# Kernel tuning notes

Hardware: AMD Instinct MI355X
Metric: run time of the kernel (lower is better)

The kernel has to match this reference:

```python
import jax, jax.numpy as jnp
import numpy as np

B, L, C, H = 8, 2048, 1024, 16
HID = 4 * C


def _rope(x):
    # Faithful to source: rotation angle depends only on feature index (no position scaling).
    b, n, c = x.shape
    k_max = c // 2
    theta = 1.0 / (10000.0 ** (jnp.arange(k_max, dtype=jnp.float32) / k_max))
    cos_t, sin_t = jnp.cos(theta), jnp.sin(theta)
    xr = x.reshape(b, n, k_max, 2)
    re = xr[..., 0] * cos_t - xr[..., 1] * sin_t
    im = xr[..., 0] * sin_t + xr[..., 1] * cos_t
    return jnp.stack((re, im), axis=-1).reshape(b, n, c)


def _dwconv(x_bcl, w, bias):
    # depthwise conv1d, kernel 3, padding 1; w: (C,1,3)
    y = jax.lax.conv_general_dilated(
        x_bcl, w, (1,), [(1, 1)],
        dimension_numbers=('NCH', 'OIH', 'NCH'),
        feature_group_count=x_bcl.shape[1])
    return y + bias[None, :, None]


def _ln(x, g, b, eps=1e-5):
    mu = x.mean(-1, keepdims=True)
    var = ((x - mu) ** 2).mean(-1, keepdims=True)
    return (x - mu) * jax.lax.rsqrt(var + eps) * g + b


def _mlla_forward(x, cpe1_w, cpe1_b, norm1_g, norm1_b, in_w, in_b, actp_w, actp_b,
                  dwc_w, dwc_b, qk_w, qk_b, lepe_w, lepe_b, out_w, out_b,
                  cpe2_w, cpe2_b, norm2_g, norm2_b, fc1_w, fc1_b, fc2_w, fc2_b):
    b, n, c = x.shape
    h, d = H, c // H
    # cpe1 residual
    x = x + _dwconv(x.transpose(0, 2, 1), cpe1_w, cpe1_b).transpose(0, 2, 1)
    shortcut = x
    xn = _ln(x, norm1_g, norm1_b)
    act_res = jax.nn.silu(xn @ actp_w + actp_b)
    xi = xn @ in_w + in_b
    xi = jax.nn.silu(_dwconv(xi.transpose(0, 2, 1), dwc_w, dwc_b)).transpose(0, 2, 1)
    # linear attention with ELU+1 feature map and RoPE on q/k
    qk = xi @ qk_w + qk_b                       # (b,n,2c)
    q = jax.nn.elu(qk[..., :c]) + 1.0
    k = jax.nn.elu(qk[..., c:]) + 1.0
    q_rope = _rope(q).reshape(b, n, h, d).transpose(0, 2, 1, 3)  # (b,h,n,d)
    k_rope = _rope(k).reshape(b, n, h, d).transpose(0, 2, 1, 3)
    qh = q.reshape(b, n, h, d).transpose(0, 2, 1, 3)
    kh = k.reshape(b, n, h, d).transpose(0, 2, 1, 3)
    vh = xi.reshape(b, n, h, d).transpose(0, 2, 1, 3)
    k_mean = kh.mean(axis=2, keepdims=True)                      # (b,h,1,d)
    z = 1.0 / (jnp.einsum('bhnd,bhmd->bhnm', qh, k_mean) + 1e-6)  # (b,h,n,1)
    kv = jnp.einsum('bhnd,bhne->bhde', k_rope, vh) * (1.0 / n)   # (k*n^-0.5)^T @ (v*n^-0.5)
    attn = jnp.einsum('bhnd,bhde->bhne', q_rope, kv) * z         # (b,h,n,d)
    attn = attn.transpose(0, 2, 1, 3).reshape(b, n, c)
    v_bcl = vh.transpose(0, 2, 1, 3).reshape(b, n, c).transpose(0, 2, 1)
    attn = attn + _dwconv(v_bcl, lepe_w, lepe_b).transpose(0, 2, 1)
    # gated output projection + residual
    x = shortcut + (attn * act_res) @ out_w + out_b
    # cpe2 residual
    x = x + _dwconv(x.transpose(0, 2, 1), cpe2_w, cpe2_b).transpose(0, 2, 1)
    # MLP (exact GELU, as torch default)
    xn2 = _ln(x, norm2_g, norm2_b)
    mlp = jax.nn.gelu(xn2 @ fc1_w + fc1_b, approximate=False) @ fc2_w + fc2_b
    return x + mlp


def setup_inputs() -> dict:
    key = jax.random.key(0)
    ks = jax.random.split(key, 12)
    def nrm(k, shape, scale=0.02):
        return jax.random.normal(k, shape, jnp.float32) * scale
    return {
        'x': jax.random.normal(ks[0], (B, L, C), jnp.float32),
        'cpe1_w': nrm(ks[1], (C, 1, 3), 0.1), 'cpe1_b': jnp.zeros((C,), jnp.float32),
        'norm1_g': jnp.ones((C,), jnp.float32), 'norm1_b': jnp.zeros((C,), jnp.float32),
        'in_w': nrm(ks[2], (C, C)), 'in_b': jnp.zeros((C,), jnp.float32),
        'actp_w': nrm(ks[3], (C, C)), 'actp_b': jnp.zeros((C,), jnp.float32),
        'dwc_w': nrm(ks[4], (C, 1, 3), 0.1), 'dwc_b': jnp.zeros((C,), jnp.float32),
        'qk_w': nrm(ks[5], (C, 2 * C)), 'qk_b': jnp.zeros((2 * C,), jnp.float32),
        'lepe_w': nrm(ks[6], (C, 1, 3), 0.1), 'lepe_b': jnp.zeros((C,), jnp.float32),
        'out_w': nrm(ks[7], (C, C)), 'out_b': jnp.zeros((C,), jnp.float32),
        'cpe2_w': nrm(ks[8], (C, 1, 3), 0.1), 'cpe2_b': jnp.zeros((C,), jnp.float32),
        'norm2_g': jnp.ones((C,), jnp.float32), 'norm2_b': jnp.zeros((C,), jnp.float32),
        'fc1_w': nrm(ks[9], (C, HID)), 'fc1_b': jnp.zeros((HID,), jnp.float32),
        'fc2_w': nrm(ks[10], (HID, C)), 'fc2_b': jnp.zeros((C,), jnp.float32),
    }


def reference(x, cpe1_w, cpe1_b, norm1_g, norm1_b, in_w, in_b, actp_w, actp_b,
              dwc_w, dwc_b, qk_w, qk_b, lepe_w, lepe_b, out_w, out_b,
              cpe2_w, cpe2_b, norm2_g, norm2_b, fc1_w, fc1_b, fc2_w, fc2_b):
    return _mlla_forward(x, cpe1_w, cpe1_b, norm1_g, norm1_b, in_w, in_b, actp_w, actp_b,
                         dwc_w, dwc_b, qk_w, qk_b, lepe_w, lepe_b, out_w, out_b,
                         cpe2_w, cpe2_b, norm2_g, norm2_b, fc1_w, fc1_b, fc2_w, fc2_b)
```

## Files before the change

### kernel.cpp

```cpp
#include <hip/hip_runtime.h>
#include <hip/hip_bf16.h>
#include <cstdint>

#define B_    8
#define L_    2048
#define C_    1024
#define H_    16
#define D_    64
#define BL_   16384
#define C2_   2048
#define HID_  4096
#define KMAX_ 512

typedef unsigned short u16;
typedef unsigned int   u32;
typedef __attribute__((ext_vector_type(8))) short short8;
typedef __attribute__((ext_vector_type(4))) float f32x4;

__device__ __forceinline__ u16 f2bf(float f){
  u32 u = __float_as_uint(f);
  u += 0x7fffu + ((u >> 16) & 1u);
  return (u16)(u >> 16);
}
__device__ __forceinline__ float bf2f(u16 v){
  return __uint_as_float(((u32)v) << 16);
}
__device__ __forceinline__ void gld16(const void* g, void* l){
  __builtin_amdgcn_global_load_lds((const __attribute__((address_space(1))) u32*)g,
                                   (__attribute__((address_space(3))) u32*)l, 16, 0, 0);
}

__global__ __launch_bounds__(256) void zerofill_kernel(float* __restrict__ p, int n){
  int i = blockIdx.x * 256 + threadIdx.x;
  if (i < n) p[i] = 0.f;
}

__global__ void rope_table_kernel(float* __restrict__ cosS, float* __restrict__ sinS){
  int t = threadIdx.x;
  if (t < KMAX_){
    float th = powf(10000.f, -(float)t / (float)KMAX_);
    cosS[t] = cosf(th);
    sinS[t] = sinf(th);
  }
}

__global__ __launch_bounds__(256) void transpose_bf16_kernel(
    const float* __restrict__ in, u16* __restrict__ out, int R, int Ccol)
{
  __shared__ float tile[32][33];
  int tx = threadIdx.x & 31, ty = threadIdx.x >> 5;
  int c = blockIdx.x * 32 + tx;
  #pragma unroll
  for (int i = 0; i < 4; ++i){
    int r = blockIdx.y * 32 + ty + i * 8;
    tile[ty + i * 8][tx] = in[(size_t)r * Ccol + c];
  }
  __syncthreads();
  int rr = blockIdx.y * 32 + tx;
  #pragma unroll
  for (int i = 0; i < 4; ++i){
    int cc = blockIdx.x * 32 + ty + i * 8;
    out[(size_t)cc * R + rr] = f2bf(tile[tx][ty + i * 8]);
  }
}

template<typename T>
__global__ __launch_bounds__(256) void cpe_ln_kernel(
    const T* __restrict__ xin, const float* __restrict__ cw, const float* __restrict__ cb,
    const float* __restrict__ g,   const float* __restrict__ beta,
    u16* __restrict__ xout, u16* __restrict__ xnout)
{
  int bl = blockIdx.x;
  int l  = bl & (L_ - 1);
  const T* xr = xin + (size_t)bl * C_;
  int t = threadIdx.x;
  float vals[4];
  float s = 0.f, ss = 0.f;
  #pragma unroll
  for (int i = 0; i < 4; ++i){
    int c = t + i * 256;
    float xm = (l > 0)      ? (float)xr[c - C_] : 0.f;
    float x0 = (float)xr[c];
    float xp = (l < L_ - 1) ? (float)xr[c + C_] : 0.f;
    float v = x0 + xm * cw[c*3] + x0 * cw[c*3+1] + xp * cw[c*3+2] + cb[c];
    vals[i] = v; s += v; ss += v * v;
  }
  int lane = t & 63, w = t >> 6;
  #pragma unroll
  for (int o = 32; o > 0; o >>= 1){ s += __shfl_down(s, o); ss += __shfl_down(ss, o); }
  __shared__ float red[8];
  __shared__ float sh[2];
  if (lane == 0){ red[w] = s; red[4 + w] = ss; }
  __syncthreads();
  if (t == 0){
    float S  = red[0] + red[1] + red[2] + red[3];
    float SS = red[4] + red[5] + red[6] + red[7];
    float mu = S * (1.f / C_);
    float var = SS * (1.f / C_) - mu * mu;
    sh[0] = mu; sh[1] = rsqrtf(var + 1e-5f);
  }
  __syncthreads();
  float mu = sh[0], inv = sh[1];
  #pragma unroll
  for (int i = 0; i < 4; ++i){
    int c = t + i * 256;
    float xn = (vals[i] - mu) * inv * g[c] + beta[c];
    xout[(size_t)bl * C_ + c]  = f2bf(vals[i]);
    xnout[(size_t)bl * C_ + c] = f2bf(xn);
  }
}
template<> __global__ __launch_bounds__(256) void cpe_ln_kernel<u16>(
    const u16* __restrict__ xin, const float* __restrict__ cw, const float* __restrict__ cb,
    const float* __restrict__ g,   const float* __restrict__ beta,
    u16* __restrict__ xout, u16* __restrict__ xnout)
{
  int bl = blockIdx.x;
  int l  = bl & (L_ - 1);
  const u16* xr = xin + (size_t)bl * C_;
  int t = threadIdx.x;
  float vals[4];
  float s = 0.f, ss = 0.f;
  #pragma unroll
  for (int i = 0; i < 4; ++i){
    int c = t + i * 256;
    float xm = (l > 0)      ? bf2f(xr[c - C_]) : 0.f;
    float x0 = bf2f(xr[c]);
    float xp = (l < L_ - 1) ? bf2f(xr[c + C_]) : 0.f;
    float v = x0 + xm * cw[c*3] + x0 * cw[c*3+1] + xp * cw[c*3+2] + cb[c];
    vals[i] = v; s += v; ss += v * v;
  }
  int lane = t & 63, w = t >> 6;
  #pragma unroll
  for (int o = 32; o > 0; o >>= 1){ s += __shfl_down(s, o); ss += __shfl_down(ss, o); }
  __shared__ float red[8];
  __shared__ float sh[2];
  if (lane == 0){ red[w] = s; red[4 + w] = ss; }
  __syncthreads();
  if (t == 0){
    float S  = red[0] + red[1] + red[2] + red[3];
    float SS = red[4] + red[5] + red[6] + red[7];
    float mu = S * (1.f / C_);
    float var = SS * (1.f / C_) - mu * mu;
    sh[0] = mu; sh[1] = rsqrtf(var + 1e-5f);
  }
  __syncthreads();
  float mu = sh[0], inv = sh[1];
  #pragma unroll
  for (int i = 0; i < 4; ++i){
    int c = t + i * 256;
    float xn = (vals[i] - mu) * inv * g[c] + beta[c];
    xout[(size_t)bl * C_ + c]  = f2bf(vals[i]);
    xnout[(size_t)bl * C_ + c] = f2bf(xn);
  }
}

__global__ __launch_bounds__(256) void dwconv_silu_kernel(
    const u16* __restrict__ xin, const float* __restrict__ w, const float* __restrict__ bias,
    u16* __restrict__ xb)
{
  int bl = blockIdx.x;
  int l  = bl & (L_ - 1);
  const u16* xr = xin + (size_t)bl * C_;
  int t = threadIdx.x;
  #pragma unroll
  for (int i = 0; i < 4; ++i){
    int c = t + i * 256;
    float xm = (l > 0)      ? bf2f(xr[c - C_]) : 0.f;
    float x0 = bf2f(xr[c]);
    float xp = (l < L_ - 1) ? bf2f(xr[c + C_]) : 0.f;
    float v = xm * w[c*3] + x0 * w[c*3+1] + xp * w[c*3+2] + bias[c];
    v = v / (1.f + expf(-v));
    xb[(size_t)bl * C_ + c] = f2bf(v);
  }
}

__global__ __launch_bounds__(256) void colmean_kernel(
    const u16* __restrict__ qkb, float* __restrict__ kmean)
{
  int chunk = blockIdx.x, b = blockIdx.y;
  int l0 = chunk * 64;
  int t = threadIdx.x;
  #pragma unroll
  for (int i = 0; i < 4; ++i){
    int c = t + i * 256;
    float s = 0.f;
    for (int r = 0; r < 64; ++r)
      s += bf2f(qkb[((size_t)(b * L_ + l0 + r)) * C2_ + C_ + c]);
    atomicAdd(&kmean[b * C_ + c], s * (1.f / (float)L_));
  }
}

__global__ __launch_bounds__(256) void z_kernel(
    const u16* __restrict__ qkb, const float* __restrict__ kmean,
    float* __restrict__ zg)
{
  int idx = blockIdx.x * 256 + threadIdx.x;
  int row = idx >> 4, h = idx & 15;
  int b = row >> 11;
  const u32* qp = (const u32*)(qkb + (size_t)row * C2_ + h * 64);
  const float2* kp = (const float2*)(kmean + b * C_ + h * 64);
  float dot = 0.f;
  #pragma unroll
  for (int i = 0; i < 32; ++i){
    u32 q2 = qp[i]; float2 k2 = kp[i];
    dot += bf2f((u16)(q2 & 0xffff)) * k2.x + bf2f((u16)(q2 >> 16)) * k2.y;
  }
  zg[idx] = 1.f / (dot + 1e-6f);
}

__global__ __launch_bounds__(256) void kv_partial_kernel(
    const u16* __restrict__ qkb, const u16* __restrict__ xi,
    const float* __restrict__ cosS, const float* __restrict__ sinS,
    float* __restrict__ part)
{
  int bh = blockIdx.x, cy = blockIdx.y;
  int b = bh >> 4, h = bh & 15;
  __shared__ float kl[8][64];
  __shared__ float vl[8][64];
  int t = threadIdx.x;
  int rs = t >> 5, j = t & 31;
  int d  = t >> 2, e0 = (t & 3) << 4;
  float cj = cosS[h * 32 + j], sj = sinS[h * 32 + j];
  float acc[16];
  #pragma unroll
  for (int e = 0; e < 16; ++e) acc[e] = 0.f;
  int l0 = cy * 512;
  for (int it = 0; it < 64; ++it){
    int l = l0 + it * 8 + rs;
    u32 kp = *(const u32*)(qkb + ((size_t)(b * L_ + l)) * C2_ + C_ + h * 64 + 2 * j);
    float k0 = bf2f((u16)(kp & 0xffff)), k1 = bf2f((u16)(kp >> 16));
    kl[rs][2*j]   = k0 * cj - k1 * sj;
    kl[rs][2*j+1] = k0 * sj + k1 * cj;
    u32 vp = *(const u32*)(xi + ((size_t)(b * L_ + l)) * C_ + h * 64 + 2 * j);
    vl[rs][2*j]   = bf2f((u16)(vp & 0xffff));
    vl[rs][2*j+1] = bf2f((u16)(vp >> 16));
    __syncthreads();
    #pragma unroll
    for (int r = 0; r < 8; ++r){
      float kd = kl[r][d];
      #pragma unroll
      for (int e = 0; e < 16; ++e) acc[e] += kd * vl[r][e0 + e];
    }
    __syncthreads();
  }
  float* po = part + ((size_t)(bh * 4 + cy)) * 4096 + d * 64 + e0;
  #pragma unroll
  for (int e = 0; e < 16; ++e) po[e] = acc[e];
}

__global__ __launch_bounds__(256) void kv_reduce_kernel(
    const float* __restrict__ part, u16* __restrict__ kvb)
{
  int bh = blockIdx.x;
  int t = threadIdx.x;
  #pragma unroll
  for (int i = 0; i < 16; ++i){
    int o = t + i * 256;
    int d = o >> 6, e = o & 63;
    float s = 0.f;
    #pragma unroll
    for (int cy = 0; cy < 4; ++cy)
      s += part[((size_t)(bh * 4 + cy)) * 4096 + o];
    kvb[(size_t)bh * 4096 + e * 64 + d] = f2bf(s * (1.f / (float)L_));
  }
}

__global__ __launch_bounds__(256, 4) void attn_kernel(
    const u16* __restrict__ qkb, const u16* __restrict__ xi,
    const u16* __restrict__ kvb, const float* __restrict__ zg,
    const float* __restrict__ cosS, const float* __restrict__ sinS,
    const float* __restrict__ lw,  const float* __restrict__ lb,
    const u16* __restrict__ actres, u16* __restrict__ gout)
{
  int rc = blockIdx.x, b = blockIdx.y, h = blockIdx.z;
  __shared__ u16 qs[64 * 64];
  int t = threadIdx.x;
  int lane = t & 63, w = t >> 6;
  int bh = b * H_ + h;
  short8 bq[4][2];
  #pragma unroll
  for (int ni = 0; ni < 4; ++ni)
    #pragma unroll
    for (int kf = 0; kf < 2; ++kf)
      bq[ni][kf] = *(const short8*)(kvb + (size_t)bh * 4096 +
                     (ni * 16 + (lane & 15)) * 64 + kf * 32 + (lane >> 4) * 8);
  int js = t & 31;
  float cj = cosS[h * 32 + js], sj = sinS[h * 32 + js];
  float w0[4], w1[4], w2[4], bb[4];
  #pragma unroll
  for (int ni = 0; ni < 4; ++ni){
    int c = h * 64 + ni * 16 + (lane & 15);
    w0[ni] = lw[c*3]; w1[ni] = lw[c*3+1]; w2[ni] = lw[c*3+2]; bb[ni] = lb[c];
  }
  for (int ch = 0; ch < 2; ++ch){
    int n0 = rc * 128 + ch * 64;
    #pragma unroll
    for (int i = 0; i < 8; ++i){
      int id = t + i * 256;
      int r = id >> 5;
      u32 q2 = *(const u32*)(qkb + ((size_t)(b * L_ + n0 + r)) * C2_ + h * 64 + 2 * js);
      float q0 = bf2f((u16)(q2 & 0xffff)), q1 = bf2f((u16)(q2 >> 16));
      u32 pk = (u32)f2bf(q0 * cj - q1 * sj) | ((u32)f2bf(q0 * sj + q1 * cj) << 16);
      *(u32*)((char*)qs + r * 128 + ((4 * js) ^ ((r & 7) << 4))) = pk;
    }
    __syncthreads();
    int arow = w * 16 + (lane & 15);
    short8 af0 = *(const short8*)((char*)qs + arow * 128 + ((     (lane >> 4) * 16) ^ ((arow & 7) << 4)));
    short8 af1 = *(const short8*)((char*)qs + arow * 128 + ((64 + (lane >> 4) * 16) ^ ((arow & 7) << 4)));
    f32x4 acc[4] = {};
    #pragma unroll
    for (int ni = 0; ni < 4; ++ni){
      acc[ni] = __builtin_amdgcn_mfma_f32_16x16x32_bf16(af0, bq[ni][0], acc[ni], 0, 0, 0);
      acc[ni] = __builtin_amdgcn_mfma_f32_16x16x32_bf16(af1, bq[ni][1], acc[ni], 0, 0, 0);
    }
    #pragma unroll
    for (int ni = 0; ni < 4; ++ni){
      int c = h * 64 + ni * 16 + (lane & 15);
      #pragma unroll
      for (int r = 0; r < 4; ++r){
        int n = n0 + w * 16 + (lane >> 4) * 4 + r;
        size_t row = (size_t)b * L_ + n;
        float attnv = acc[ni][r] * zg[(row << 4) + h];
        float vm = (n > 0)      ? bf2f(xi[(row - 1) * C_ + c]) : 0.f;
        float v0 = bf2f(xi[row * C_ + c]);
        float vp = (n < L_ - 1) ? bf2f(xi[(row + 1) * C_ + c]) : 0.f;
        float gval = (attnv + vm * w0[ni] + v0 * w1[ni] + vp * w2[ni] + bb[ni]) * bf2f(actres[row * C_ + c]);
        gout[row * C_ + c] = f2bf(gval);
      }
    }
    __syncthreads();
  }
}

enum { EP_SILU = 0, EP_NONE = 1, EP_ELU1 = 2, EP_RES_BF = 3, EP_GELU = 4, EP_RES_F32 = 5 };

template<int EP>
__global__ __launch_bounds__(256) void gemm_bf16(
    const u16* __restrict__ A,
    const u16* __restrict__ Bt,
    const float* __restrict__ bias,
    const u16* __restrict__ res,
    float* __restrict__ outF, u16* __restrict__ outB,
    int M, int N, int K)
{
  __shared__ u16 As[128 * 64];
  __shared__ u16 Bs[128 * 64];
  const int t = threadIdx.x;
  const int m0 = blockIdx.x * 128;
  const int n0 = blockIdx.y * 128;
  const int lane = t & 63, w = t >> 6;
  const int wm = (w >> 1) * 64, wn = (w & 1) * 64;
  f32x4 acc[4][4] = {};
  const int ktiles = K >> 6;
  const int sidx = t;
  for (int kt = 0; kt < ktiles; ++kt){
    const u16* Ab = A  + (size_t)m0 * K + kt * 64;
    const u16* Bb = Bt + (size_t)n0 * K + kt * 64;
    #pragma unroll
    for (int i = 0; i < 4; ++i){
      int idx = sidx + i * 256;
      int row = idx >> 3, k8 = idx & 7;
      int srcoff = row * K + ((k8 * 8) ^ ((row & 7) << 3));
      int wb = (i * 256 + (t & 192)) * 8;
      gld16(Ab + srcoff, &As[wb]);
      gld16(Bb + srcoff, &Bs[wb]);
    }
    __syncthreads();
    #pragma unroll
    for (int ks = 0; ks < 2; ++ks){
      short8 af[4], bfr[4];
      int kk = ks * 32 + ((lane >> 4) << 3);
      #pragma unroll
      for (int mi = 0; mi < 4; ++mi){
        int row = wm + mi * 16 + (lane & 15);
        af[mi] = *(const short8*)(&As[row * 64 + (kk ^ ((row & 7) << 3))]);
      }
      #pragma unroll
      for (int ni = 0; ni < 4; ++ni){
        int row = wn + ni * 16 + (lane & 15);
        bfr[ni] = *(const short8*)(&Bs[row * 64 + (kk ^ ((row & 7) << 3))]);
      }
      #pragma unroll
      for (int mi = 0; mi < 4; ++mi)
        #pragma unroll
        for (int ni = 0; ni < 4; ++ni)
          acc[mi][ni] = __builtin_amdgcn_mfma_f32_16x16x32_bf16(af[mi], bfr[ni], acc[mi][ni], 0, 0, 0);
    }
    __syncthreads();
  }
  #pragma unroll
  for (int mi = 0; mi < 4; ++mi){
    #pragma unroll
    for (int ni = 0; ni < 4; ++ni){
      int gmb = m0 + wm + mi * 16 + ((lane >> 4) << 2);
      int gn  = n0 + wn + ni * 16 + (lane & 15);
      float bv = bias[gn];
      #pragma unroll
      for (int r = 0; r < 4; ++r){
        int gm = gmb + r;
        float v = acc[mi][ni][r] + bv;
        size_t o = (size_t)gm * N + gn;
        if (EP == EP_SILU)      outB[o] = f2bf(v / (1.f + expf(-v)));
        else if (EP == EP_NONE) outB[o] = f2bf(v);
        else if (EP == EP_ELU1) outB[o] = f2bf((v > 0.f) ? (v + 1.f) : expf(v));
        else if (EP == EP_RES_BF) outB[o] = f2bf(v + bf2f(res[o]));
        else if (EP == EP_GELU) outB[o] = f2bf(0.5f * v * (1.f + erff(v * 0.70710678118f)));
        else if (EP == EP_RES_F32) outF[o] = v + bf2f(res[o]);
      }
    }
  }
}

extern "C" void kernel_launch(void* const* d_in, const int* in_sizes, int n_in,
                              void* d_out, int out_size, void* d_ws, size_t ws_size,
                              hipStream_t stream)
{
  const float* x       = (const float*)d_in[0];
  const float* cpe1_w  = (const float*)d_in[1];
  const float* cpe1_b  = (const float*)d_in[2];
  const float* norm1_g = (const float*)d_in[3];
  const float* norm1_b = (const float*)d_in[4];
  const float* in_w    = (const float*)d_in[5];
  const float* in_b    = (const float*)d_in[6];
  const float* actp_w  = (const float*)d_in[7];
  const float* actp_b  = (const float*)d_in[8];
  const float* dwc_w   = (const float*)d_in[9];
  const float* dwc_b   = (const float*)d_in[10];
  const float* qk_w    = (const float*)d_in[11];
  const float* qk_b    = (const float*)d_in[12];
  const float* lepe_w  = (const float*)d_in[13];
  const float* lepe_b  = (const float*)d_in[14];
  const float* out_w   = (const float*)d_in[15];
  const float* out_b   = (const float*)d_in[16];
  const float* cpe2_w  = (const float*)d_in[17];
  const float* cpe2_b  = (const float*)d_in[18];
  const float* norm2_g = (const float*)d_in[19];
  const float* norm2_b = (const float*)d_in[20];
  const float* fc1_w   = (const float*)d_in[21];
  const float* fc1_b   = (const float*)d_in[22];
  const float* fc2_w   = (const float*)d_in[23];
  const float* fc2_b   = (const float*)d_in[24];
  float* out = (float*)d_out;

  char* ws = (char*)d_ws;
  size_t off = 0;
  auto alloc = [&](size_t bytes) -> char* {
    char* p = ws + off;
    off = (off + bytes + 255) & ~(size_t)255;
    return p;
  };
  float* cosS   = (float*)alloc(KMAX_ * 4);
  float* sinS   = (float*)alloc(KMAX_ * 4);
  u16* wTactp   = (u16*)alloc((size_t)C_ * C_ * 2);
  u16* wTin     = (u16*)alloc((size_t)C_ * C_ * 2);
  u16* wTqk     = (u16*)alloc((size_t)C2_ * C_ * 2);
  u16* wTout    = (u16*)alloc((size_t)C_ * C_ * 2);
  u16* wTfc1    = (u16*)alloc((size_t)HID_ * C_ * 2);
  u16* wTfc2    = (u16*)alloc((size_t)C_ * HID_ * 2);
  float* kmean  = (float*)alloc((size_t)B_ * C_ * 4);
  u16*   kvb    = (u16*)alloc((size_t)128 * 4096 * 2);
  float* kvpart = (float*)alloc((size_t)512 * 4096 * 4);
  float* zbuf   = (float*)alloc((size_t)BL_ * H_ * 4);
  u16* x1       = (u16*)alloc((size_t)BL_ * C_ * 2);
  u16* bufX     = (u16*)alloc((size_t)BL_ * C_ * 2);
  u16* bufY     = (u16*)alloc((size_t)BL_ * C_ * 2);
  u16* bufW     = (u16*)alloc((size_t)BL_ * C_ * 2);
  u16* bufQ     = (u16*)alloc((size_t)BL_ * C2_ * 2);
  size_t needed = off;
  if (ws_size < needed) return;

  u16* xi0 = bufQ;
  u16* qkb = bufQ;
  u16* x2  = bufQ;
  u16* xi  = bufW;
  u16* hb  = bufW;
  u16* actres = bufY;
  u16* x3  = bufY;

  rope_table_kernel<<<1, 512, 0, stream>>>(cosS, sinS);
  transpose_bf16_kernel<<<dim3(C_/32,  C_/32 ), 256, 0, stream>>>(actp_w, wTactp, C_,  C_);
  transpose_bf16_kernel<<<dim3(C_/32,  C_/32 ), 256, 0, stream>>>(in_w,   wTin,   C_,  C_);
  transpose_bf16_kernel<<<dim3(C2_/32, C_/32 ), 256, 0, stream>>>(qk_w,   wTqk,   C_,  C2_);
  transpose_bf16_kernel<<<dim3(C_/32,  C_/32 ), 256, 0, stream>>>(out_w,  wTout,  C_,  C_);
  transpose_bf16_kernel<<<dim3(HID_/32,C_/32 ), 256, 0, stream>>>(fc1_w,  wTfc1,  C_,  HID_);
  transpose_bf16_kernel<<<dim3(C_/32,  HID_/32), 256, 0, stream>>>(fc2_w,  wTfc2,  HID_, C_);
  zerofill_kernel<<<(B_*C_ + 255)/256, 256, 0, stream>>>(kmean, B_*C_);

  cpe_ln_kernel<float><<<BL_, 256, 0, stream>>>(x, cpe1_w, cpe1_b, norm1_g, norm1_b, x1, bufX);
  gemm_bf16<EP_SILU><<<dim3(BL_/128, C_/128), 256, 0, stream>>>(
      bufX, wTactp, actp_b, nullptr, nullptr, actres, BL_, C_, C_);
  gemm_bf16<EP_NONE><<<dim3(BL_/128, C_/128), 256, 0, stream>>>(
      bufX, wTin, in_b, nullptr, nullptr, xi0, BL_, C_, C_);
  dwconv_silu_kernel<<<BL_, 256, 0, stream>>>(xi0, dwc_w, dwc_b, xi);
  gemm_bf16<EP_ELU1><<<dim3(BL_/128, C2_/128), 256, 0, stream>>>(
      xi, wTqk, qk_b, nullptr, nullptr, qkb, BL_, C2_, C_);
  colmean_kernel<<<dim3(32, B_), 256, 0, stream>>>(qkb, kmean);
  z_kernel<<<BL_*H_/256, 256, 0, stream>>>(qkb, kmean, zbuf);
  kv_partial_kernel<<<dim3(128, 4), 256, 0, stream>>>(qkb, xi, cosS, sinS, kvpart);
  kv_reduce_kernel<<<128, 256, 0, stream>>>(kvpart, kvb);
  attn_kernel<<<dim3(16, B_, H_), 256, 0, stream>>>(
      qkb, xi, kvb, zbuf, cosS, sinS, lepe_w, lepe_b, actres, bufX);
  gemm_bf16<EP_RES_BF><<<dim3(BL_/128, C_/128), 256, 0, stream>>>(
      bufX, wTout, out_b, x1, nullptr, x2, BL_, C_, C_);
  cpe_ln_kernel<u16><<<BL_, 256, 0, stream>>>(x2, cpe2_w, cpe2_b, norm2_g, norm2_b, x3, bufX);
  for (int m = 0; m < 4; ++m){
    size_t ro = (size_t)m * 4096;
    gemm_bf16<EP_GELU><<<dim3(32, HID_/128), 256, 0, stream>>>(
        bufX + ro * C_, wTfc1, fc1_b, nullptr, nullptr, hb, 4096, HID_, C_);
    gemm_bf16<EP_RES_F32><<<dim3(32, C_/128), 256, 0, stream>>>(
        hb, wTfc2, fc2_b, x3 + ro * C_, out + ro * C_, nullptr, 4096, C_, HID_);
  }
}
```

Before: 1.324 ms.

## Use 32x32 MFMA tiles, fuse act/in projections, approximate GELU with tanh-form

The GEMM inner loop moves from 16x16x32 MFMA with a 4x4 fragment grid to 32x32x16 MFMA with a 2x2 grid, which cuts LDS fragment reads and instruction count per k-step. The act-projection and input-projection GEMMs are merged into one N=2048 GEMM over concatenated transposed weights and biases, with a split epilogue writing SiLU and plain outputs to two buffers. The erf-based GELU epilogue is replaced by a sigmoid/tanh approximation, which is cheaper but changes numerics slightly.

```diff
diff --git a/kernel.cpp b/kernel.cpp
--- a/kernel.cpp
+++ b/kernel.cpp
@@ -16,6 +16,7 @@
 typedef unsigned int   u32;
 typedef __attribute__((ext_vector_type(8))) short short8;
 typedef __attribute__((ext_vector_type(4))) float f32x4;
+typedef __attribute__((ext_vector_type(16))) float f32x16;
 
 __device__ __forceinline__ u16 f2bf(float f){
   u32 u = __float_as_uint(f);
@@ -33,6 +34,13 @@
 __global__ __launch_bounds__(256) void zerofill_kernel(float* __restrict__ p, int n){
   int i = blockIdx.x * 256 + threadIdx.x;
   if (i < n) p[i] = 0.f;
+}
+
+__global__ __launch_bounds__(256) void concat_bias_kernel(
+    const float* __restrict__ b0, const float* __restrict__ b1, float* __restrict__ o){
+  int i = blockIdx.x * 256 + threadIdx.x;
+  if (i < C_) o[i] = b0[i];
+  else if (i < C2_) o[i] = b1[i - C_];
 }
 
 __global__ void rope_table_kernel(float* __restrict__ cosS, float* __restrict__ sinS){
@@ -332,7 +340,7 @@
   }
 }
 
-enum { EP_SILU = 0, EP_NONE = 1, EP_ELU1 = 2, EP_RES_BF = 3, EP_GELU = 4, EP_RES_F32 = 5 };
+enum { EP_SILU = 0, EP_NONE = 1, EP_ELU1 = 2, EP_RES_BF = 3, EP_GELU = 4, EP_RES_F32 = 5, EP_ACTIN = 6 };
 
 template<int EP>
 __global__ __launch_bounds__(256) void gemm_bf16(
@@ -340,7 +348,7 @@
     const u16* __restrict__ Bt,
     const float* __restrict__ bias,
     const u16* __restrict__ res,
-    float* __restrict__ outF, u16* __restrict__ outB,
+    float* __restrict__ outF, u16* __restrict__ outB, u16* __restrict__ outB2,
     int M, int N, int K)
 {
   __shared__ u16 As[128 * 64];
@@ -350,15 +358,14 @@
   const int n0 = blockIdx.y * 128;
   const int lane = t & 63, w = t >> 6;
   const int wm = (w >> 1) * 64, wn = (w & 1) * 64;
-  f32x4 acc[4][4] = {};
+  f32x16 acc00 = {}, acc01 = {}, acc10 = {}, acc11 = {};
   const int ktiles = K >> 6;
-  const int sidx = t;
   for (int kt = 0; kt < ktiles; ++kt){
     const u16* Ab = A  + (size_t)m0 * K + kt * 64;
     const u16* Bb = Bt + (size_t)n0 * K + kt * 64;
     #pragma unroll
     for (int i = 0; i < 4; ++i){
-      int idx = sidx + i * 256;
+      int idx = t + i * 256;
       int row = idx >> 3, k8 = idx & 7;
       int srcoff = row * K + ((k8 * 8) ^ ((row & 7) << 3));
       int wb = (i * 256 + (t & 192)) * 8;
@@ -366,46 +373,50 @@
       gld16(Bb + srcoff, &Bs[wb]);
     }
     __syncthreads();
-    #pragma unroll
-    for (int ks = 0; ks < 2; ++ks){
-      short8 af[4], bfr[4];
-      int kk = ks * 32 + ((lane >> 4) << 3);
-      #pragma unroll
-      for (int mi = 0; mi < 4; ++mi){
-        int row = wm + mi * 16 + (lane & 15);
-        af[mi] = *(const short8*)(&As[row * 64 + (kk ^ ((row & 7) << 3))]);
-      }
-      #pragma unroll
-      for (int ni = 0; ni < 4; ++ni){
-        int row = wn + ni * 16 + (lane & 15);
-        bfr[ni] = *(const short8*)(&Bs[row * 64 + (kk ^ ((row & 7) << 3))]);
-      }
-      #pragma unroll
-      for (int mi = 0; mi < 4; ++mi)
-        #pragma unroll
-        for (int ni = 0; ni < 4; ++ni)
-          acc[mi][ni] = __builtin_amdgcn_mfma_f32_16x16x32_bf16(af[mi], bfr[ni], acc[mi][ni], 0, 0, 0);
+    const int rA0 = wm + (lane & 31), rA1 = rA0 + 32;
+    const int rB0 = wn + (lane & 31), rB1 = rB0 + 32;
+    const int sw = (lane & 7) << 3;
+    #pragma unroll
+    for (int ks = 0; ks < 4; ++ks){
+      int kb = ks * 16 + ((lane >> 5) << 3);
+      short8 a0 = *(const short8*)(&As[rA0 * 64 + (kb ^ sw)]);
+      short8 a1 = *(const short8*)(&As[rA1 * 64 + (kb ^ sw)]);
+      short8 b0 = *(const short8*)(&Bs[rB0 * 64 + (kb ^ sw)]);
+      short8 b1 = *(const short8*)(&Bs[rB1 * 64 + (kb ^ sw)]);
+      acc00 = __builtin_amdgcn_mfma_f32_32x32x16_bf16(a0, b0, acc00, 0, 0, 0);
+      acc01 = __builtin_amdgcn_mfma_f32_32x32x16_bf16(a0, b1, acc01, 0, 0, 0);
+      acc10 = __builtin_amdgcn_mfma_f32_32x32x16_bf16(a1, b0, acc10, 0, 0, 0);
+      acc11 = __builtin_amdgcn_mfma_f32_32x32x16_bf16(a1, b1, acc11, 0, 0, 0);
     }
     __syncthreads();
   }
-  #pragma unroll
-  for (int mi = 0; mi < 4; ++mi){
-    #pragma unroll
-    for (int ni = 0; ni < 4; ++ni){
-      int gmb = m0 + wm + mi * 16 + ((lane >> 4) << 2);
-      int gn  = n0 + wn + ni * 16 + (lane & 15);
+  const int rbase = (lane >> 5) << 2;
+  #pragma unroll
+  for (int mi = 0; mi < 2; ++mi){
+    #pragma unroll
+    for (int ni = 0; ni < 2; ++ni){
+      const f32x16& a = (mi == 0) ? (ni == 0 ? acc00 : acc01) : (ni == 0 ? acc10 : acc11);
+      int gn = n0 + wn + ni * 32 + (lane & 31);
       float bv = bias[gn];
       #pragma unroll
-      for (int r = 0; r < 4; ++r){
-        int gm = gmb + r;
-        float v = acc[mi][ni][r] + bv;
+      for (int r = 0; r < 16; ++r){
+        int gm = m0 + wm + mi * 32 + (r & 3) + ((r >> 2) << 3) + rbase;
+        float v = a[r] + bv;
         size_t o = (size_t)gm * N + gn;
         if (EP == EP_SILU)      outB[o] = f2bf(v / (1.f + expf(-v)));
         else if (EP == EP_NONE) outB[o] = f2bf(v);
         else if (EP == EP_ELU1) outB[o] = f2bf((v > 0.f) ? (v + 1.f) : expf(v));
         else if (EP == EP_RES_BF) outB[o] = f2bf(v + bf2f(res[o]));
-        else if (EP == EP_GELU) outB[o] = f2bf(0.5f * v * (1.f + erff(v * 0.70710678118f)));
+        else if (EP == EP_GELU){
+          float u = v * (1.5957691f + 0.0713549f * v * v);
+          outB[o] = f2bf(v / (1.f + expf(-u)));
+        }
         else if (EP == EP_RES_F32) outF[o] = v + bf2f(res[o]);
+        else if (EP == EP_ACTIN){
+          int half = N >> 1;
+          if (gn < half) outB[(size_t)gm * half + gn] = f2bf(v / (1.f + expf(-v)));
+          else           outB2[(size_t)gm * half + gn - half] = f2bf(v);
+        }
       }
     }
   }
@@ -451,12 +462,12 @@
   };
   float* cosS   = (float*)alloc(KMAX_ * 4);
   float* sinS   = (float*)alloc(KMAX_ * 4);
-  u16* wTactp   = (u16*)alloc((size_t)C_ * C_ * 2);
-  u16* wTin     = (u16*)alloc((size_t)C_ * C_ * 2);
+  u16* wTai     = (u16*)alloc((size_t)2 * C_ * C_ * 2);
   u16* wTqk     = (u16*)alloc((size_t)C2_ * C_ * 2);
   u16* wTout    = (u16*)alloc((size_t)C_ * C_ * 2);
   u16* wTfc1    = (u16*)alloc((size_t)HID_ * C_ * 2);
   u16* wTfc2    = (u16*)alloc((size_t)C_ * HID_ * 2);
+  float* biasAI = (float*)alloc((size_t)C2_ * 4);
   float* kmean  = (float*)alloc((size_t)B_ * C_ * 4);
   u16*   kvb    = (u16*)alloc((size_t)128 * 4096 * 2);
   float* kvpart = (float*)alloc((size_t)512 * 4096 * 4);
@@ -469,6 +480,8 @@
   size_t needed = off;
   if (ws_size < needed) return;
 
+  u16* wTactp = wTai;
+  u16* wTin   = wTai + (size_t)C_ * C_;
   u16* xi0 = bufQ;
   u16* qkb = bufQ;
   u16* x2  = bufQ;
@@ -484,16 +497,15 @@
   transpose_bf16_kernel<<<dim3(C_/32,  C_/32 ), 256, 0, stream>>>(out_w,  wTout,  C_,  C_);
   transpose_bf16_kernel<<<dim3(HID_/32,C_/32 ), 256, 0, stream>>>(fc1_w,  wTfc1,  C_,  HID_);
   transpose_bf16_kernel<<<dim3(C_/32,  HID_/32), 256, 0, stream>>>(fc2_w,  wTfc2,  HID_, C_);
+  concat_bias_kernel<<<C2_/256, 256, 0, stream>>>(actp_b, in_b, biasAI);
   zerofill_kernel<<<(B_*C_ + 255)/256, 256, 0, stream>>>(kmean, B_*C_);
 
   cpe_ln_kernel<float><<<BL_, 256, 0, stream>>>(x, cpe1_w, cpe1_b, norm1_g, norm1_b, x1, bufX);
-  gemm_bf16<EP_SILU><<<dim3(BL_/128, C_/128), 256, 0, stream>>>(
-      bufX, wTactp, actp_b, nullptr, nullptr, actres, BL_, C_, C_);
-  gemm_bf16<EP_NONE><<<dim3(BL_/128, C_/128), 256, 0, stream>>>(
-      bufX, wTin, in_b, nullptr, nullptr, xi0, BL_, C_, C_);
+  gemm_bf16<EP_ACTIN><<<dim3(BL_/128, C2_/128), 256, 0, stream>>>(
+      bufX, wTai, biasAI, nullptr, nullptr, actres, xi0, BL_, C2_, C_);
   dwconv_silu_kernel<<<BL_, 256, 0, stream>>>(xi0, dwc_w, dwc_b, xi);
   gemm_bf16<EP_ELU1><<<dim3(BL_/128, C2_/128), 256, 0, stream>>>(
-      xi, wTqk, qk_b, nullptr, nullptr, qkb, BL_, C2_, C_);
+      xi, wTqk, qk_b, nullptr, nullptr, qkb, nullptr, BL_, C2_, C_);
   colmean_kernel<<<dim3(32, B_), 256, 0, stream>>>(qkb, kmean);
   z_kernel<<<BL_*H_/256, 256, 0, stream>>>(qkb, kmean, zbuf);
   kv_partial_kernel<<<dim3(128, 4), 256, 0, stream>>>(qkb, xi, cosS, sinS, kvpart);
@@ -501,13 +513,13 @@
   attn_kernel<<<dim3(16, B_, H_), 256, 0, stream>>>(
       qkb, xi, kvb, zbuf, cosS, sinS, lepe_w, lepe_b, actres, bufX);
   gemm_bf16<EP_RES_BF><<<dim3(BL_/128, C_/128), 256, 0, stream>>>(
-      bufX, wTout, out_b, x1, nullptr, x2, BL_, C_, C_);
+      bufX, wTout, out_b, x1, nullptr, x2, nullptr, BL_, C_, C_);
   cpe_ln_kernel<u16><<<BL_, 256, 0, stream>>>(x2, cpe2_w, cpe2_b, norm2_g, norm2_b, x3, bufX);
   for (int m = 0; m < 4; ++m){
     size_t ro = (size_t)m * 4096;
     gemm_bf16<EP_GELU><<<dim3(32, HID_/128), 256, 0, stream>>>(
-        bufX + ro * C_, wTfc1, fc1_b, nullptr, nullptr, hb, 4096, HID_, C_);
+        bufX + ro * C_, wTfc1, fc1_b, nullptr, nullptr, hb, nullptr, 4096, HID_, C_);
     gemm_bf16<EP_RES_F32><<<dim3(32, C_/128), 256, 0, stream>>>(
-        hb, wTfc2, fc2_b, x3 + ro * C_, out + ro * C_, nullptr, 4096, C_, HID_);
-  }
-}
+        hb, wTfc2, fc2_b, x3 + ro * C_, out + ro * C_, nullptr, nullptr, 4096, C_, HID_);
+  }
+}
```

After: 1.260 ms. 1.05x faster.
